# Kernel tuning notes

Measured on AMD Instinct MI355X. Metric: run time of the kernel, lower is better.

Reference implementation:

```python
import jax, jax.numpy as jnp
import numpy as np

DIN = 256
HID = 512

def setup_inputs() -> dict:
    key = jax.random.key(0)
    ks = jax.random.split(key, 9)
    s_in = 1.0 / np.sqrt(DIN)
    s_h = 1.0 / np.sqrt(HID)
    h = jax.random.normal(ks[0], (32, 1024, DIN), dtype=jnp.float32)
    Wv = jax.random.uniform(ks[1], (HID, DIN), jnp.float32, -s_in, s_in)
    bv = jax.random.uniform(ks[2], (HID,), jnp.float32, -s_in, s_in)
    Wk = jax.random.uniform(ks[3], (HID, DIN), jnp.float32, -s_in, s_in)
    bk = jax.random.uniform(ks[4], (HID,), jnp.float32, -s_in, s_in)
    Wq = jax.random.uniform(ks[5], (HID, DIN), jnp.float32, -s_in, s_in)
    bq = jax.random.uniform(ks[6], (HID,), jnp.float32, -s_in, s_in)
    Wo = jax.random.uniform(ks[7], (DIN, HID), jnp.float32, -s_h, s_h)
    bo = jax.random.uniform(ks[8], (DIN,), jnp.float32, -s_h, s_h)
    return {"h": h, "Wv": Wv, "bv": bv, "Wk": Wk, "bk": bk, "Wq": Wq, "bq": bq, "Wo": Wo, "bo": bo}

def reference(h, Wv, bv, Wk, bk, Wq, bq, Wo, bo):
    # relu-activated Q/K/V projections: [B, N, HID]
    v = jax.nn.relu(jnp.einsum('bnd,hd->bnh', h, Wv) + bv)
    q = jax.nn.relu(jnp.einsum('bnd,hd->bnh', h, Wq) + bq)
    k = jax.nn.relu(jnp.einsum('bnd,hd->bnh', h, Wk) + bk)
    # unscaled attention: [B, N, N]
    att = jax.nn.softmax(jnp.einsum('bnh,bmh->bnm', q, k), axis=2)
    out = jnp.einsum('bnm,bmh->bnh', att, v)          # [B, N, HID]
    out = jax.nn.relu(jnp.einsum('bnh,dh->bnd', out, Wo) + bo)  # [B, N, DIN]
    return out
```

## Files before the change

kernel.cpp:

```cpp
#include <hip/hip_runtime.h>
#include <cstdint>
#include <cstddef>

#define NB    32
#define SEQ   1024
#define DIN   256
#define HID   512
#define MTOT  32768

typedef _Float16 half_t;
typedef _Float16 half8  __attribute__((ext_vector_type(8)));
typedef _Float16 half4v __attribute__((ext_vector_type(4)));
typedef float    f32x4  __attribute__((ext_vector_type(4)));

typedef __attribute__((address_space(1))) const void* gas_ptr;
typedef __attribute__((address_space(3))) void*       las_ptr;

__global__ void cvt_kernel(const float* __restrict__ src, half_t* __restrict__ dst, int n4) {
    int i = blockIdx.x * blockDim.x + threadIdx.x;
    if (i < n4) {
        f32x4 v = ((const f32x4*)src)[i];
        half4v h;
        h[0] = (half_t)v[0]; h[1] = (half_t)v[1]; h[2] = (half_t)v[2]; h[3] = (half_t)v[3];
        ((half4v*)dst)[i] = h;
    }
}

__global__ void cvt4_kernel(const float* __restrict__ s0, const float* __restrict__ s1,
                            const float* __restrict__ s2, const float* __restrict__ s3,
                            half_t* __restrict__ d0, half_t* __restrict__ d1,
                            half_t* __restrict__ d2, half_t* __restrict__ d3, int n4) {
    int y = blockIdx.y;
    const float* s = y == 0 ? s0 : y == 1 ? s1 : y == 2 ? s2 : s3;
    half_t*      d = y == 0 ? d0 : y == 1 ? d1 : y == 2 ? d2 : d3;
    int i = blockIdx.x * blockDim.x + threadIdx.x;
    if (i < n4) {
        f32x4 v = ((const f32x4*)s)[i];
        half4v h;
        h[0] = (half_t)v[0]; h[1] = (half_t)v[1]; h[2] = (half_t)v[2]; h[3] = (half_t)v[3];
        ((half4v*)d)[i] = h;
    }
}

__global__ void pack_bias(const float* __restrict__ bv, const float* __restrict__ bk,
                          const float* __restrict__ bq, float* __restrict__ dst) {
    int t = threadIdx.x;
    if (t < HID) {
        dst[t]         = bv[t];
        dst[HID + t]   = bk[t];
        dst[2*HID + t] = bq[t];
    }
}

template<int MODE>
__global__ __launch_bounds__(256, 2) void gemm_k(
    const half_t* __restrict__ A, long lda, long a_bs,
    const half_t* __restrict__ Bw, long ldb, long b_bs,
    void* __restrict__ Out, long ldo, long o_bs,
    const float* __restrict__ bias,
    int Kdim, half_t* __restrict__ out2)
{
    __shared__ alignas(16) half_t As[128 * 32];
    __shared__ alignas(16) half_t Bs[128 * 32];

    const int t    = threadIdx.x;
    const int lane = t & 63;
    const int wave = t >> 6;
    const int wm   = wave >> 1;
    const int wn   = wave & 1;
    const int lanen = lane & 15;
    const int quad  = lane >> 4;
    const int z     = blockIdx.z;
    const long m0 = (long)blockIdx.x * 128;
    const long n0 = (long)blockIdx.y * 128;

    const half_t* Ab = A  + (long)z * a_bs;
    const half_t* Bb = Bw + (long)z * b_bs;

    f32x4 acc[4][4];
#pragma unroll
    for (int i = 0; i < 4; i++)
#pragma unroll
        for (int j = 0; j < 4; j++)
            acc[i][j] = f32x4{0.f, 0.f, 0.f, 0.f};

    const int c0 = t, c1 = t + 256;
    const int r0 = c0 >> 2, kc0 = c0 & 3;
    const int r1 = c1 >> 2, kc1 = c1 & 3;

    const half_t* gA0 = Ab + (m0 + r0) * lda + kc0 * 8;
    const half_t* gA1 = Ab + (m0 + r1) * lda + kc1 * 8;
    const half_t* gB0 = Bb + (n0 + r0) * ldb + kc0 * 8;
    const half_t* gB1 = Bb + (n0 + r1) * ldb + kc1 * 8;
    half_t* lA0 = &As[c0 * 8];
    half_t* lA1 = &As[c1 * 8];
    half_t* lB0 = &Bs[c0 * 8];
    half_t* lB1 = &Bs[c1 * 8];

    int aoff[4], boff[4];
#pragma unroll
    for (int i = 0; i < 4; i++) aoff[i] = (wm * 64 + i * 16 + lanen) * 32 + quad * 8;
#pragma unroll
    for (int j = 0; j < 4; j++) boff[j] = (wn * 64 + j * 16 + lanen) * 32 + quad * 8;

    for (int k0 = 0; k0 < Kdim; k0 += 32) {
        __builtin_amdgcn_global_load_lds((gas_ptr)(gA0 + k0), (las_ptr)lA0, 16, 0, 0);
        __builtin_amdgcn_global_load_lds((gas_ptr)(gA1 + k0), (las_ptr)lA1, 16, 0, 0);
        __builtin_amdgcn_global_load_lds((gas_ptr)(gB0 + k0), (las_ptr)lB0, 16, 0, 0);
        __builtin_amdgcn_global_load_lds((gas_ptr)(gB1 + k0), (las_ptr)lB1, 16, 0, 0);
        __syncthreads();

        half8 af[4], bf[4];
#pragma unroll
        for (int i = 0; i < 4; i++) af[i] = *(const half8*)&As[aoff[i]];
#pragma unroll
        for (int j = 0; j < 4; j++) bf[j] = *(const half8*)&Bs[boff[j]];
#pragma unroll
        for (int i = 0; i < 4; i++)
#pragma unroll
            for (int j = 0; j < 4; j++)
                acc[i][j] = __builtin_amdgcn_mfma_f32_16x16x32_f16(af[i], bf[j], acc[i][j], 0, 0, 0);
        __syncthreads();
    }

#pragma unroll
    for (int i = 0; i < 4; i++) {
        long mrow = m0 + wm * 64 + i * 16 + quad * 4;
#pragma unroll
        for (int j = 0; j < 4; j++) {
            long gn = n0 + wn * 64 + j * 16 + lanen;
            f32x4 v = acc[i][j];
            if (MODE == 0) {
                float bb = bias[z * HID + gn];
                half_t h0 = (half_t)fmaxf(v[0] + bb, 0.f);
                half_t h1 = (half_t)fmaxf(v[1] + bb, 0.f);
                half_t h2 = (half_t)fmaxf(v[2] + bb, 0.f);
                half_t h3 = (half_t)fmaxf(v[3] + bb, 0.f);
                if (z == 0) {
                    long bidx = mrow >> 10;
                    long pos  = mrow & 1023;
                    half4v pk; pk[0] = h0; pk[1] = h1; pk[2] = h2; pk[3] = h3;
                    *(half4v*)(out2 + ((bidx * HID + gn) << 10) + pos) = pk;
                } else {
                    half_t* o = (half_t*)Out + (long)(z - 1) * o_bs;
                    o[(mrow + 0) * ldo + gn] = h0;
                    o[(mrow + 1) * ldo + gn] = h1;
                    o[(mrow + 2) * ldo + gn] = h2;
                    o[(mrow + 3) * ldo + gn] = h3;
                }
            } else {
                float* o = (float*)Out;
                float bb = bias[gn];
#pragma unroll
                for (int r = 0; r < 4; r++) o[(mrow + r) * ldo + gn] = fmaxf(v[r] + bb, 0.f);
            }
        }
    }
}

__global__ __launch_bounds__(256, 2) void se_k(
    const half_t* __restrict__ Q, const half_t* __restrict__ K,
    half_t* __restrict__ E, float* __restrict__ Mstat, float* __restrict__ Lstat)
{
    __shared__ alignas(16) half_t As[128 * 32];
    __shared__ alignas(16) half_t Bs[256 * 32];

    const int t    = threadIdx.x;
    const int lane = t & 63;
    const int wave = t >> 6;
    const int wm   = wave >> 1;
    const int wn   = wave & 1;
    const int lanen = lane & 15;
    const int quad  = lane >> 4;
    const int z     = blockIdx.z;
    const long m0 = (long)blockIdx.x * 128;
    const long n0 = (long)blockIdx.y * 256;

    const half_t* Ab = Q + (long)z * SEQ * HID;
    const half_t* Bb = K + (long)z * SEQ * HID;

    f32x4 acc[4][8];
#pragma unroll
    for (int i = 0; i < 4; i++)
#pragma unroll
        for (int j = 0; j < 8; j++)
            acc[i][j] = f32x4{0.f, 0.f, 0.f, 0.f};

    const half_t* gA[2]; half_t* lA[2];
    const half_t* gB[4]; half_t* lB[4];
#pragma unroll
    for (int s = 0; s < 2; s++) {
        int c = t + 256 * s;
        gA[s] = Ab + (m0 + (c >> 2)) * HID + (c & 3) * 8;
        lA[s] = &As[c * 8];
    }
#pragma unroll
    for (int s = 0; s < 4; s++) {
        int c = t + 256 * s;
        gB[s] = Bb + (n0 + (c >> 2)) * HID + (c & 3) * 8;
        lB[s] = &Bs[c * 8];
    }

    int aoff[4], boff[8];
#pragma unroll
    for (int i = 0; i < 4; i++) aoff[i] = (wm * 64 + i * 16 + lanen) * 32 + quad * 8;
#pragma unroll
    for (int j = 0; j < 8; j++) boff[j] = (wn * 128 + j * 16 + lanen) * 32 + quad * 8;

    for (int k0 = 0; k0 < HID; k0 += 32) {
#pragma unroll
        for (int s = 0; s < 2; s++)
            __builtin_amdgcn_global_load_lds((gas_ptr)(gA[s] + k0), (las_ptr)lA[s], 16, 0, 0);
#pragma unroll
        for (int s = 0; s < 4; s++)
            __builtin_amdgcn_global_load_lds((gas_ptr)(gB[s] + k0), (las_ptr)lB[s], 16, 0, 0);
        __syncthreads();

        half8 af[4], bf[8];
#pragma unroll
        for (int i = 0; i < 4; i++) af[i] = *(const half8*)&As[aoff[i]];
#pragma unroll
        for (int j = 0; j < 8; j++) bf[j] = *(const half8*)&Bs[boff[j]];
#pragma unroll
        for (int i = 0; i < 4; i++)
#pragma unroll
            for (int j = 0; j < 8; j++)
                acc[i][j] = __builtin_amdgcn_mfma_f32_16x16x32_f16(af[i], bf[j], acc[i][j], 0, 0, 0);
        __syncthreads();
    }

    float mf[4][4];
#pragma unroll
    for (int i = 0; i < 4; i++)
#pragma unroll
        for (int r = 0; r < 4; r++) {
            float v = acc[i][0][r];
#pragma unroll
            for (int j = 1; j < 8; j++) v = fmaxf(v, acc[i][j][r]);
#pragma unroll
            for (int off = 8; off > 0; off >>= 1)
                v = fmaxf(v, __shfl_xor(v, off, 64));
            mf[i][r] = v;
        }

    half_t* Eb = E + (long)z * SEQ * SEQ;
    float rs[4][4];
#pragma unroll
    for (int i = 0; i < 4; i++)
#pragma unroll
        for (int r = 0; r < 4; r++) rs[i][r] = 0.f;
#pragma unroll
    for (int i = 0; i < 4; i++) {
        long mrow = m0 + wm * 64 + i * 16 + quad * 4;
#pragma unroll
        for (int j = 0; j < 8; j++) {
            long gn = n0 + wn * 128 + j * 16 + lanen;
#pragma unroll
            for (int r = 0; r < 4; r++) {
                float e = __expf(acc[i][j][r] - mf[i][r]);
                rs[i][r] += e;
                Eb[(mrow + r) * SEQ + gn] = (half_t)e;
            }
        }
    }
#pragma unroll
    for (int i = 0; i < 4; i++)
#pragma unroll
        for (int r = 0; r < 4; r++) {
            float v = rs[i][r];
#pragma unroll
            for (int off = 8; off > 0; off >>= 1)
                v += __shfl_xor(v, off, 64);
            rs[i][r] = v;
        }

    if (lanen == 0) {
        long base = ((long)z * 8 + blockIdx.y * 2 + wn) * SEQ + m0 + wm * 64;
#pragma unroll
        for (int i = 0; i < 4; i++)
#pragma unroll
            for (int r = 0; r < 4; r++) {
                Mstat[base + i * 16 + quad * 4 + r] = mf[i][r];
                Lstat[base + i * 16 + quad * 4 + r] = rs[i][r];
            }
    }
}

__global__ __launch_bounds__(256, 2) void pv_k(
    const half_t* __restrict__ E, const half_t* __restrict__ vT,
    const float* __restrict__ Mstat, const float* __restrict__ Lstat,
    half_t* __restrict__ O16)
{
    __shared__ alignas(16) half_t As[128 * 32];
    __shared__ alignas(16) half_t Bs[256 * 32];
    __shared__ float scaleS[8][128];
    __shared__ float invS[128];

    const int t    = threadIdx.x;
    const int lane = t & 63;
    const int wave = t >> 6;
    const int wm   = wave >> 1;
    const int wn   = wave & 1;
    const int lanen = lane & 15;
    const int quad  = lane >> 4;
    const int z     = blockIdx.z;
    const long m0 = (long)blockIdx.x * 128;
    const long h0 = (long)blockIdx.y * 256;

    if (t < 128) {
        float mv[8];
        float M = -1e30f;
#pragma unroll
        for (int kb = 0; kb < 8; kb++) {
            mv[kb] = Mstat[((long)z * 8 + kb) * SEQ + m0 + t];
            M = fmaxf(M, mv[kb]);
        }
        float ls = 0.f;
#pragma unroll
        for (int kb = 0; kb < 8; kb++) {
            float sc = __expf(mv[kb] - M);
            scaleS[kb][t] = sc;
            ls += Lstat[((long)z * 8 + kb) * SEQ + m0 + t] * sc;
        }
        invS[t] = 1.f / ls;
    }
    __syncthreads();

    const half_t* Ab = E  + (long)z * SEQ * SEQ;
    const half_t* Bb = vT + (long)z * HID * SEQ;

    f32x4 acc[4][8];
#pragma unroll
    for (int i = 0; i < 4; i++)
#pragma unroll
        for (int j = 0; j < 8; j++)
            acc[i][j] = f32x4{0.f, 0.f, 0.f, 0.f};

    const half_t* gA[2]; half_t* lA[2];
    const half_t* gB[4]; half_t* lB[4];
#pragma unroll
    for (int s = 0; s < 2; s++) {
        int c = t + 256 * s;
        gA[s] = Ab + (m0 + (c >> 2)) * SEQ + (c & 3) * 8;
        lA[s] = &As[c * 8];
    }
#pragma unroll
    for (int s = 0; s < 4; s++) {
        int c = t + 256 * s;
        gB[s] = Bb + (h0 + (c >> 2)) * SEQ + (c & 3) * 8;
        lB[s] = &Bs[c * 8];
    }

    int aoff[4], boff[8];
#pragma unroll
    for (int i = 0; i < 4; i++) aoff[i] = (wm * 64 + i * 16 + lanen) * 32 + quad * 8;
#pragma unroll
    for (int j = 0; j < 8; j++) boff[j] = (wn * 128 + j * 16 + lanen) * 32 + quad * 8;

    for (int k0 = 0; k0 < SEQ; k0 += 32) {
#pragma unroll
        for (int s = 0; s < 2; s++)
            __builtin_amdgcn_global_load_lds((gas_ptr)(gA[s] + k0), (las_ptr)lA[s], 16, 0, 0);
#pragma unroll
        for (int s = 0; s < 4; s++)
            __builtin_amdgcn_global_load_lds((gas_ptr)(gB[s] + k0), (las_ptr)lB[s], 16, 0, 0);
        __syncthreads();

        const int kb = k0 >> 7;
        half8 af[4], bf[8];
#pragma unroll
        for (int i = 0; i < 4; i++) {
            af[i] = *(const half8*)&As[aoff[i]];
            half_t sh = (half_t)scaleS[kb][wm * 64 + i * 16 + lanen];
            af[i] *= sh;
        }
#pragma unroll
        for (int j = 0; j < 8; j++) bf[j] = *(const half8*)&Bs[boff[j]];
#pragma unroll
        for (int i = 0; i < 4; i++)
#pragma unroll
            for (int j = 0; j < 8; j++)
                acc[i][j] = __builtin_amdgcn_mfma_f32_16x16x32_f16(af[i], bf[j], acc[i][j], 0, 0, 0);
        __syncthreads();
    }

    half_t* o = O16 + (long)z * SEQ * HID;
#pragma unroll
    for (int i = 0; i < 4; i++) {
        long mrow = m0 + wm * 64 + i * 16 + quad * 4;
        int rl = wm * 64 + i * 16 + quad * 4;
#pragma unroll
        for (int j = 0; j < 8; j++) {
            long gn = h0 + wn * 128 + j * 16 + lanen;
#pragma unroll
            for (int r = 0; r < 4; r++)
                o[(mrow + r) * HID + gn] = (half_t)(acc[i][j][r] * invS[rl + r]);
        }
    }
}

extern "C" void kernel_launch(void* const* d_in, const int* in_sizes, int n_in,
                              void* d_out, int out_size, void* d_ws, size_t ws_size,
                              hipStream_t stream) {
    const float* h  = (const float*)d_in[0];
    const float* Wv = (const float*)d_in[1];
    const float* bv = (const float*)d_in[2];
    const float* Wk = (const float*)d_in[3];
    const float* bk = (const float*)d_in[4];
    const float* Wq = (const float*)d_in[5];
    const float* bq = (const float*)d_in[6];
    const float* Wo = (const float*)d_in[7];
    const float* bo = (const float*)d_in[8];

    uint8_t* ws = (uint8_t*)d_ws;
    size_t off = 0;
    auto alloc = [&](size_t bytes) { size_t o = off; off += (bytes + 255) & ~(size_t)255; return o; };

    half_t* W16   = (half_t*)(ws + alloc((size_t)3 * HID * DIN * 2));
    half_t* Wo16  = (half_t*)(ws + alloc((size_t)DIN * HID * 2));
    float*  biasq = (float*)(ws + alloc((size_t)3 * HID * 4));
    half_t* k16   = (half_t*)(ws + alloc((size_t)MTOT * HID * 2));
    half_t* q16   = (half_t*)(ws + alloc((size_t)MTOT * HID * 2));
    half_t* vT    = (half_t*)(ws + alloc((size_t)MTOT * HID * 2));
    size_t h16_off = alloc((size_t)MTOT * DIN * 2);
    half_t* h16   = (half_t*)(ws + h16_off);
    half_t* O16 = q16;

    size_t s_avail = ws_size > h16_off ? ws_size - h16_off : 0;
    size_t per_batch = (size_t)SEQ * SEQ * 2 + 2 * 8 * SEQ * 4;
    int GB = (int)(s_avail / per_batch);
    if (GB < 1)  GB = 1;
    if (GB > NB) GB = NB;
    half_t* Ebuf  = (half_t*)(ws + h16_off);
    float*  Mstat = (float*)(ws + h16_off + (size_t)GB * SEQ * SEQ * 2);
    float*  Lstat = Mstat + (size_t)GB * 8 * SEQ;

    cvt_kernel<<<dim3((MTOT * DIN / 4 + 255) / 256), 256, 0, stream>>>(h, h16, MTOT * DIN / 4);
    cvt4_kernel<<<dim3((HID * DIN / 4 + 255) / 256, 4), 256, 0, stream>>>(
        Wv, Wk, Wq, Wo, W16, W16 + HID * DIN, W16 + 2 * HID * DIN, Wo16, HID * DIN / 4);
    pack_bias<<<dim3(1), 512, 0, stream>>>(bv, bk, bq, biasq);

    gemm_k<0><<<dim3(MTOT / 128, HID / 128, 3), 256, 0, stream>>>(
        h16, DIN, 0,
        W16, DIN, (long)HID * DIN,
        (void*)k16, HID, (long)MTOT * HID,
        biasq, DIN, vT);

    for (int g0 = 0; g0 < NB; g0 += GB) {
        int gb = NB - g0 < GB ? NB - g0 : GB;
        se_k<<<dim3(SEQ / 128, SEQ / 256, gb), 256, 0, stream>>>(
            q16 + (size_t)g0 * SEQ * HID,
            k16 + (size_t)g0 * SEQ * HID,
            Ebuf, Mstat, Lstat);
        pv_k<<<dim3(SEQ / 128, HID / 256, gb), 256, 0, stream>>>(
            Ebuf, vT + (size_t)g0 * HID * SEQ,
            Mstat, Lstat,
            O16 + (size_t)g0 * SEQ * HID);
    }

    gemm_k<3><<<dim3(MTOT / 128, DIN / 128, 1), 256, 0, stream>>>(
        O16, HID, 0,
        Wo16, HID, 0,
        d_out, DIN, 0,
        bo, HID, nullptr);

    (void)in_sizes; (void)n_in; (void)out_size;
}
```

Before: 293.5 us.

## Fuse score and PV kernels into single flash-attention kernel with online softmax

Replaces the two-pass attention (score kernel writing a full exp-score matrix plus per-block stats, then a PV kernel rescaling and multiplying by V) with one flash-style kernel. Each 512-thread block owns 128 query rows of one batch, streams K and V in 256-key tiles through double-buffered LDS, keeps the probabilities in swizzled LDS, and applies online max/sum rescaling to the output accumulator. This removes the large HBM round trip of the score matrix and the batch-group loop, at the cost of 134KB of LDS per block, many block-wide barriers, and only 256 blocks in the grid. The output is written in place over Q, which is safe only if each block finishes reading its own Q rows before overwriting them.

Result: slower. 408.4 us (+39.1%).

```diff
diff --git a/kernel.cpp b/kernel.cpp
--- a/kernel.cpp
+++ b/kernel.cpp
@@ -158,243 +158,232 @@
     }
 }
 
-__global__ __launch_bounds__(256, 2) void se_k(
-    const half_t* __restrict__ Q, const half_t* __restrict__ K,
-    half_t* __restrict__ E, float* __restrict__ Mstat, float* __restrict__ Lstat)
+
+#define STAGE_S(dst, kv0, ho)                                                          \
+    do {                                                                               \
+        __builtin_amdgcn_global_load_lds((gas_ptr)(Qb + (long)qrow * HID + (ho) + qc * 8), \
+                                         (las_ptr)((dst) + t * 8), 16, 0, 0);          \
+        half_t* kd_ = (dst) + 4096;                                                    \
+        _Pragma("unroll")                                                              \
+        for (int s2 = 0; s2 < 2; s2++) {                                               \
+            int idx_ = t + 512 * s2;                                                   \
+            __builtin_amdgcn_global_load_lds(                                          \
+                (gas_ptr)(Kb + (long)((kv0) + (idx_ >> 2)) * HID + (ho) + (idx_ & 3) * 8), \
+                (las_ptr)(kd_ + idx_ * 8), 16, 0, 0);                                  \
+        }                                                                              \
+    } while (0)
+
+#define STAGE_V(dst, kv0, kc)                                                          \
+    do {                                                                               \
+        _Pragma("unroll")                                                              \
+        for (int s2 = 0; s2 < 4; s2++) {                                               \
+            int idx_ = t + 512 * s2;                                                   \
+            __builtin_amdgcn_global_load_lds(                                          \
+                (gas_ptr)(Vb + (long)(idx_ >> 2) * SEQ + (kv0) + (kc) * 32 + (idx_ & 3) * 8), \
+                (las_ptr)((dst) + idx_ * 8), 16, 0, 0);                                \
+        }                                                                              \
+    } while (0)
+
+__global__ __launch_bounds__(512, 2) void flash_k(
+    const half_t* Q, const half_t* __restrict__ K,
+    const half_t* __restrict__ vT, half_t* O)
 {
-    __shared__ alignas(16) half_t As[128 * 32];
-    __shared__ alignas(16) half_t Bs[256 * 32];
-
-    const int t    = threadIdx.x;
-    const int lane = t & 63;
-    const int wave = t >> 6;
-    const int wm   = wave >> 1;
-    const int wn   = wave & 1;
+    __shared__ alignas(16) unsigned char SM[137216];
+    half_t* Uh   = (half_t*)SM;
+    half_t* Ps   = (half_t*)(SM + 65536);
+    float*  m_s  = (float*)(SM + 131072);
+    float*  l_s  = (float*)(SM + 131072 + 512);
+    float*  al_s = (float*)(SM + 131072 + 1024);
+    float*  mn_s = (float*)(SM + 131072 + 1536);
+    float*  pm   = (float*)(SM + 131072 + 2048);
+    float*  psum = (float*)(SM + 131072 + 4096);
+
+    half_t* sb[2] = { Uh, Uh + 20480 };
+    half_t* vb[2] = { Uh, Uh + 16384 };
+
+    const int t     = threadIdx.x;
+    const int lane  = t & 63;
+    const int wv    = t >> 6;
+    const int wA    = wv & 1;
+    const int wB    = wv >> 1;
     const int lanen = lane & 15;
     const int quad  = lane >> 4;
-    const int z     = blockIdx.z;
-    const long m0 = (long)blockIdx.x * 128;
-    const long n0 = (long)blockIdx.y * 256;
-
-    const half_t* Ab = Q + (long)z * SEQ * HID;
-    const half_t* Bb = K + (long)z * SEQ * HID;
-
-    f32x4 acc[4][8];
-#pragma unroll
-    for (int i = 0; i < 4; i++)
-#pragma unroll
-        for (int j = 0; j < 8; j++)
-            acc[i][j] = f32x4{0.f, 0.f, 0.f, 0.f};
-
-    const half_t* gA[2]; half_t* lA[2];
-    const half_t* gB[4]; half_t* lB[4];
-#pragma unroll
-    for (int s = 0; s < 2; s++) {
-        int c = t + 256 * s;
-        gA[s] = Ab + (m0 + (c >> 2)) * HID + (c & 3) * 8;
-        lA[s] = &As[c * 8];
-    }
-#pragma unroll
-    for (int s = 0; s < 4; s++) {
-        int c = t + 256 * s;
-        gB[s] = Bb + (n0 + (c >> 2)) * HID + (c & 3) * 8;
-        lB[s] = &Bs[c * 8];
-    }
-
-    int aoff[4], boff[8];
-#pragma unroll
-    for (int i = 0; i < 4; i++) aoff[i] = (wm * 64 + i * 16 + lanen) * 32 + quad * 8;
-#pragma unroll
-    for (int j = 0; j < 8; j++) boff[j] = (wn * 128 + j * 16 + lanen) * 32 + quad * 8;
-
-    for (int k0 = 0; k0 < HID; k0 += 32) {
-#pragma unroll
-        for (int s = 0; s < 2; s++)
-            __builtin_amdgcn_global_load_lds((gas_ptr)(gA[s] + k0), (las_ptr)lA[s], 16, 0, 0);
-#pragma unroll
-        for (int s = 0; s < 4; s++)
-            __builtin_amdgcn_global_load_lds((gas_ptr)(gB[s] + k0), (las_ptr)lB[s], 16, 0, 0);
+
+    const int bid = blockIdx.x;
+    const int z   = (bid & 7) + 8 * ((bid >> 3) & 3);
+    const long m0 = (long)(bid >> 5) * 128;
+
+    const half_t* Qb = Q  + (long)z * SEQ * HID + m0 * HID;
+    const half_t* Kb = K  + (long)z * SEQ * HID;
+    const half_t* Vb = vT + (long)z * HID * SEQ;
+    half_t*       Ob = O  + (long)z * SEQ * HID + m0 * HID;
+
+    const int qrow = t >> 2, qc = t & 3;
+
+    if (t < 128) { m_s[t] = -1e30f; l_s[t] = 0.f; }
+
+    f32x4 acc2[8][4];
+#pragma unroll
+    for (int a = 0; a < 8; a++)
+#pragma unroll
+        for (int b = 0; b < 4; b++) acc2[a][b] = f32x4{0.f,0.f,0.f,0.f};
+
+    const int pswz_r = ((lanen & 3) << 4) ^ (((lanen >> 2) & 3) << 5);
+    const int wmaskq = quad << 5;
+
+    STAGE_S(sb[0], 0, 0);
+    __syncthreads();
+
+    for (int kt = 0; kt < 4; kt++) {
+        const int kv0 = kt * 256;
+
+        f32x4 acc[4][4];
+#pragma unroll
+        for (int i = 0; i < 4; i++)
+#pragma unroll
+            for (int jj = 0; jj < 4; jj++) acc[i][jj] = f32x4{0.f,0.f,0.f,0.f};
+
+        for (int c = 0; c < 16; c++) {
+            if (c < 15) STAGE_S(sb[(c + 1) & 1], kv0, (c + 1) * 32);
+            else        STAGE_V(vb[0], kv0, 0);
+            const half_t* Qc = sb[c & 1];
+            const half_t* Kc = sb[c & 1] + 4096;
+            half8 bf[4];
+#pragma unroll
+            for (int jj = 0; jj < 4; jj++)
+                bf[jj] = *(const half8*)&Kc[(wB * 64 + jj * 16 + lanen) * 32 + quad * 8];
+#pragma unroll
+            for (int i = 0; i < 4; i++) {
+                half8 af = *(const half8*)&Qc[(wA * 64 + i * 16 + lanen) * 32 + quad * 8];
+#pragma unroll
+                for (int jj = 0; jj < 4; jj++)
+                    acc[i][jj] = __builtin_amdgcn_mfma_f32_16x16x32_f16(af, bf[jj], acc[i][jj], 0, 0, 0);
+            }
+            __syncthreads();
+        }
+
+#pragma unroll
+        for (int i = 0; i < 4; i++) {
+            float px[4];
+#pragma unroll
+            for (int rr = 0; rr < 4; rr++) {
+                float v = fmaxf(fmaxf(acc[i][0][rr], acc[i][1][rr]),
+                                fmaxf(acc[i][2][rr], acc[i][3][rr]));
+                v = fmaxf(v, __shfl_xor(v, 1, 64));
+                v = fmaxf(v, __shfl_xor(v, 2, 64));
+                v = fmaxf(v, __shfl_xor(v, 4, 64));
+                v = fmaxf(v, __shfl_xor(v, 8, 64));
+                px[rr] = v;
+            }
+            if (lanen == 0) {
+#pragma unroll
+                for (int rr = 0; rr < 4; rr++)
+                    pm[(wA * 64 + i * 16 + quad * 4 + rr) * 4 + wB] = px[rr];
+            }
+        }
         __syncthreads();
 
-        half8 af[4], bf[8];
-#pragma unroll
-        for (int i = 0; i < 4; i++) af[i] = *(const half8*)&As[aoff[i]];
-#pragma unroll
-        for (int j = 0; j < 8; j++) bf[j] = *(const half8*)&Bs[boff[j]];
-#pragma unroll
-        for (int i = 0; i < 4; i++)
-#pragma unroll
-            for (int j = 0; j < 8; j++)
-                acc[i][j] = __builtin_amdgcn_mfma_f32_16x16x32_f16(af[i], bf[j], acc[i][j], 0, 0, 0);
+#pragma unroll
+        for (int i = 0; i < 4; i++) {
+            float mn_[4], al_[4], sm_[4];
+#pragma unroll
+            for (int rr = 0; rr < 4; rr++) {
+                int row = wA * 64 + i * 16 + quad * 4 + rr;
+                f32x4 p4 = *(const f32x4*)&pm[row * 4];
+                float tm = fmaxf(fmaxf(p4[0], p4[1]), fmaxf(p4[2], p4[3]));
+                float mo = m_s[row];
+                float mn = fmaxf(mo, tm);
+                mn_[rr] = mn;
+                al_[rr] = __expf(mo - mn);
+                sm_[rr] = 0.f;
+            }
+#pragma unroll
+            for (int jj = 0; jj < 4; jj++) {
+                int col = wB * 64 + jj * 16 + lanen;
+#pragma unroll
+                for (int rr = 0; rr < 4; rr++) {
+                    float e = __expf(acc[i][jj][rr] - mn_[rr]);
+                    sm_[rr] += e;
+                    int q = wA * 64 + i * 16 + quad * 4 + rr;
+                    int byteoff = q * 512 + ((col * 2) ^ (rr << 4) ^ wmaskq);
+                    *(half_t*)((unsigned char*)Ps + byteoff) = (half_t)e;
+                }
+            }
+#pragma unroll
+            for (int rr = 0; rr < 4; rr++) {
+                float v = sm_[rr];
+                v += __shfl_xor(v, 1, 64);
+                v += __shfl_xor(v, 2, 64);
+                v += __shfl_xor(v, 4, 64);
+                v += __shfl_xor(v, 8, 64);
+                sm_[rr] = v;
+            }
+            if (lanen == 0) {
+#pragma unroll
+                for (int rr = 0; rr < 4; rr++) {
+                    int row = wA * 64 + i * 16 + quad * 4 + rr;
+                    psum[row * 4 + wB] = sm_[rr];
+                    if (wB == 0) { al_s[row] = al_[rr]; mn_s[row] = mn_[rr]; }
+                }
+            }
+        }
         __syncthreads();
-    }
-
-    float mf[4][4];
-#pragma unroll
-    for (int i = 0; i < 4; i++)
-#pragma unroll
-        for (int r = 0; r < 4; r++) {
-            float v = acc[i][0][r];
-#pragma unroll
-            for (int j = 1; j < 8; j++) v = fmaxf(v, acc[i][j][r]);
-#pragma unroll
-            for (int off = 8; off > 0; off >>= 1)
-                v = fmaxf(v, __shfl_xor(v, off, 64));
-            mf[i][r] = v;
-        }
-
-    half_t* Eb = E + (long)z * SEQ * SEQ;
-    float rs[4][4];
-#pragma unroll
-    for (int i = 0; i < 4; i++)
-#pragma unroll
-        for (int r = 0; r < 4; r++) rs[i][r] = 0.f;
-#pragma unroll
-    for (int i = 0; i < 4; i++) {
-        long mrow = m0 + wm * 64 + i * 16 + quad * 4;
-#pragma unroll
-        for (int j = 0; j < 8; j++) {
-            long gn = n0 + wn * 128 + j * 16 + lanen;
-#pragma unroll
-            for (int r = 0; r < 4; r++) {
-                float e = __expf(acc[i][j][r] - mf[i][r]);
-                rs[i][r] += e;
-                Eb[(mrow + r) * SEQ + gn] = (half_t)e;
-            }
-        }
-    }
-#pragma unroll
-    for (int i = 0; i < 4; i++)
-#pragma unroll
-        for (int r = 0; r < 4; r++) {
-            float v = rs[i][r];
-#pragma unroll
-            for (int off = 8; off > 0; off >>= 1)
-                v += __shfl_xor(v, off, 64);
-            rs[i][r] = v;
-        }
-
-    if (lanen == 0) {
-        long base = ((long)z * 8 + blockIdx.y * 2 + wn) * SEQ + m0 + wm * 64;
-#pragma unroll
-        for (int i = 0; i < 4; i++)
-#pragma unroll
-            for (int r = 0; r < 4; r++) {
-                Mstat[base + i * 16 + quad * 4 + r] = mf[i][r];
-                Lstat[base + i * 16 + quad * 4 + r] = rs[i][r];
-            }
-    }
-}
-
-__global__ __launch_bounds__(256, 2) void pv_k(
-    const half_t* __restrict__ E, const half_t* __restrict__ vT,
-    const float* __restrict__ Mstat, const float* __restrict__ Lstat,
-    half_t* __restrict__ O16)
-{
-    __shared__ alignas(16) half_t As[128 * 32];
-    __shared__ alignas(16) half_t Bs[256 * 32];
-    __shared__ float scaleS[8][128];
-    __shared__ float invS[128];
-
-    const int t    = threadIdx.x;
-    const int lane = t & 63;
-    const int wave = t >> 6;
-    const int wm   = wave >> 1;
-    const int wn   = wave & 1;
-    const int lanen = lane & 15;
-    const int quad  = lane >> 4;
-    const int z     = blockIdx.z;
-    const long m0 = (long)blockIdx.x * 128;
-    const long h0 = (long)blockIdx.y * 256;
-
-    if (t < 128) {
-        float mv[8];
-        float M = -1e30f;
-#pragma unroll
-        for (int kb = 0; kb < 8; kb++) {
-            mv[kb] = Mstat[((long)z * 8 + kb) * SEQ + m0 + t];
-            M = fmaxf(M, mv[kb]);
-        }
-        float ls = 0.f;
-#pragma unroll
-        for (int kb = 0; kb < 8; kb++) {
-            float sc = __expf(mv[kb] - M);
-            scaleS[kb][t] = sc;
-            ls += Lstat[((long)z * 8 + kb) * SEQ + m0 + t] * sc;
-        }
-        invS[t] = 1.f / ls;
-    }
-    __syncthreads();
-
-    const half_t* Ab = E  + (long)z * SEQ * SEQ;
-    const half_t* Bb = vT + (long)z * HID * SEQ;
-
-    f32x4 acc[4][8];
-#pragma unroll
-    for (int i = 0; i < 4; i++)
-#pragma unroll
-        for (int j = 0; j < 8; j++)
-            acc[i][j] = f32x4{0.f, 0.f, 0.f, 0.f};
-
-    const half_t* gA[2]; half_t* lA[2];
-    const half_t* gB[4]; half_t* lB[4];
-#pragma unroll
-    for (int s = 0; s < 2; s++) {
-        int c = t + 256 * s;
-        gA[s] = Ab + (m0 + (c >> 2)) * SEQ + (c & 3) * 8;
-        lA[s] = &As[c * 8];
-    }
-#pragma unroll
-    for (int s = 0; s < 4; s++) {
-        int c = t + 256 * s;
-        gB[s] = Bb + (h0 + (c >> 2)) * SEQ + (c & 3) * 8;
-        lB[s] = &Bs[c * 8];
-    }
-
-    int aoff[4], boff[8];
-#pragma unroll
-    for (int i = 0; i < 4; i++) aoff[i] = (wm * 64 + i * 16 + lanen) * 32 + quad * 8;
-#pragma unroll
-    for (int j = 0; j < 8; j++) boff[j] = (wn * 128 + j * 16 + lanen) * 32 + quad * 8;
-
-    for (int k0 = 0; k0 < SEQ; k0 += 32) {
-#pragma unroll
-        for (int s = 0; s < 2; s++)
-            __builtin_amdgcn_global_load_lds((gas_ptr)(gA[s] + k0), (las_ptr)lA[s], 16, 0, 0);
-#pragma unroll
-        for (int s = 0; s < 4; s++)
-            __builtin_amdgcn_global_load_lds((gas_ptr)(gB[s] + k0), (las_ptr)lB[s], 16, 0, 0);
-        __syncthreads();
-
-        const int kb = k0 >> 7;
-        half8 af[4], bf[8];
-#pragma unroll
-        for (int i = 0; i < 4; i++) {
-            af[i] = *(const half8*)&As[aoff[i]];
-            half_t sh = (half_t)scaleS[kb][wm * 64 + i * 16 + lanen];
-            af[i] *= sh;
-        }
-#pragma unroll
-        for (int j = 0; j < 8; j++) bf[j] = *(const half8*)&Bs[boff[j]];
-#pragma unroll
-        for (int i = 0; i < 4; i++)
-#pragma unroll
-            for (int j = 0; j < 8; j++)
-                acc[i][j] = __builtin_amdgcn_mfma_f32_16x16x32_f16(af[i], bf[j], acc[i][j], 0, 0, 0);
-        __syncthreads();
-    }
-
-    half_t* o = O16 + (long)z * SEQ * HID;
-#pragma unroll
-    for (int i = 0; i < 4; i++) {
-        long mrow = m0 + wm * 64 + i * 16 + quad * 4;
-        int rl = wm * 64 + i * 16 + quad * 4;
-#pragma unroll
-        for (int j = 0; j < 8; j++) {
-            long gn = h0 + wn * 128 + j * 16 + lanen;
-#pragma unroll
-            for (int r = 0; r < 4; r++)
-                o[(mrow + r) * HID + gn] = (half_t)(acc[i][j][r] * invS[rl + r]);
+
+        if (wB == 0 && lanen == 0) {
+#pragma unroll
+            for (int i = 0; i < 4; i++)
+#pragma unroll
+                for (int rr = 0; rr < 4; rr++) {
+                    int row = wA * 64 + i * 16 + quad * 4 + rr;
+                    f32x4 s4 = *(const f32x4*)&psum[row * 4];
+                    l_s[row] = l_s[row] * al_s[row] + (s4[0] + s4[1] + s4[2] + s4[3]);
+                    m_s[row] = mn_s[row];
+                }
+        }
+
+#pragma unroll
+        for (int b = 0; b < 4; b++) {
+            float al = al_s[wA * 64 + b * 16 + lanen];
+#pragma unroll
+            for (int a = 0; a < 8; a++) {
+                acc2[a][b][0] *= al; acc2[a][b][1] *= al;
+                acc2[a][b][2] *= al; acc2[a][b][3] *= al;
+            }
+        }
+
+        for (int kc = 0; kc < 8; kc++) {
+            if (kc < 7)      STAGE_V(vb[(kc + 1) & 1], kv0, kc + 1);
+            else if (kt < 3) STAGE_S(sb[0], kv0 + 256, 0);
+            const half_t* Vc = vb[kc & 1];
+            half8 pf[4];
+#pragma unroll
+            for (int b = 0; b < 4; b++) {
+                int q = wA * 64 + b * 16 + lanen;
+                int byteoff = q * 512 + ((kc * 64 + quad * 16) ^ pswz_r);
+                pf[b] = *(const half8*)((const unsigned char*)Ps + byteoff);
+            }
+#pragma unroll
+            for (int a = 0; a < 8; a++) {
+                half8 vf = *(const half8*)&Vc[(wB * 128 + a * 16 + lanen) * 32 + quad * 8];
+#pragma unroll
+                for (int b = 0; b < 4; b++)
+                    acc2[a][b] = __builtin_amdgcn_mfma_f32_16x16x32_f16(vf, pf[b], acc2[a][b], 0, 0, 0);
+            }
+            __syncthreads();
+        }
+    }
+
+#pragma unroll
+    for (int b = 0; b < 4; b++) {
+        long qg = wA * 64 + b * 16 + lanen;
+        float inv = 1.f / l_s[qg];
+#pragma unroll
+        for (int a = 0; a < 8; a++) {
+            f32x4 v = acc2[a][b];
+            half4v pk;
+            pk[0] = (half_t)(v[0] * inv); pk[1] = (half_t)(v[1] * inv);
+            pk[2] = (half_t)(v[2] * inv); pk[3] = (half_t)(v[3] * inv);
+            *(half4v*)&Ob[qg * HID + wB * 128 + a * 16 + quad * 4] = pk;
         }
     }
 }
@@ -422,18 +411,7 @@
     half_t* k16   = (half_t*)(ws + alloc((size_t)MTOT * HID * 2));
     half_t* q16   = (half_t*)(ws + alloc((size_t)MTOT * HID * 2));
     half_t* vT    = (half_t*)(ws + alloc((size_t)MTOT * HID * 2));
-    size_t h16_off = alloc((size_t)MTOT * DIN * 2);
-    half_t* h16   = (half_t*)(ws + h16_off);
-    half_t* O16 = q16;
-
-    size_t s_avail = ws_size > h16_off ? ws_size - h16_off : 0;
-    size_t per_batch = (size_t)SEQ * SEQ * 2 + 2 * 8 * SEQ * 4;
-    int GB = (int)(s_avail / per_batch);
-    if (GB < 1)  GB = 1;
-    if (GB > NB) GB = NB;
-    half_t* Ebuf  = (half_t*)(ws + h16_off);
-    float*  Mstat = (float*)(ws + h16_off + (size_t)GB * SEQ * SEQ * 2);
-    float*  Lstat = Mstat + (size_t)GB * 8 * SEQ;
+    half_t* h16   = (half_t*)(ws + alloc((size_t)MTOT * DIN * 2));
 
     cvt_kernel<<<dim3((MTOT * DIN / 4 + 255) / 256), 256, 0, stream>>>(h, h16, MTOT * DIN / 4);
     cvt4_kernel<<<dim3((HID * DIN / 4 + 255) / 256, 4), 256, 0, stream>>>(
@@ -446,23 +424,13 @@
         (void*)k16, HID, (long)MTOT * HID,
         biasq, DIN, vT);
 
-    for (int g0 = 0; g0 < NB; g0 += GB) {
-        int gb = NB - g0 < GB ? NB - g0 : GB;
-        se_k<<<dim3(SEQ / 128, SEQ / 256, gb), 256, 0, stream>>>(
-            q16 + (size_t)g0 * SEQ * HID,
-            k16 + (size_t)g0 * SEQ * HID,
-            Ebuf, Mstat, Lstat);
-        pv_k<<<dim3(SEQ / 128, HID / 256, gb), 256, 0, stream>>>(
-            Ebuf, vT + (size_t)g0 * HID * SEQ,
-            Mstat, Lstat,
-            O16 + (size_t)g0 * SEQ * HID);
-    }
+    flash_k<<<dim3(NB * (SEQ / 128)), dim3(512), 0, stream>>>(q16, k16, vT, q16);
 
     gemm_k<3><<<dim3(MTOT / 128, DIN / 128, 1), 256, 0, stream>>>(
-        O16, HID, 0,
+        q16, HID, 0,
         Wo16, HID, 0,
         d_out, DIN, 0,
         bo, HID, nullptr);
 
-    (void)in_sizes; (void)n_in; (void)out_size;
-}
+    (void)in_sizes; (void)n_in; (void)out_size; (void)ws_size;
+}
```
